# Kernel optimization log

Hardware: AMD Instinct MI355X
Metric: run time of the kernel (lower is better)

Reference implementation:

```python
import jax, jax.numpy as jnp
import numpy as np

M, K, N = 8192, 4096, 4096


def setup_inputs() -> dict:
    key = jax.random.key(0)
    k1, k2, k3 = jax.random.split(key, 3)
    inp = jax.random.normal(k1, (M, K), dtype=jnp.float32)
    weight = jax.random.normal(k2, (N, K), dtype=jnp.float32)
    bias = jax.random.normal(k3, (N,), dtype=jnp.bfloat16)
    return {"inp": inp, "weight": weight, "bias": bias}


def reference(inp, weight, bias):
    # FP8TensorMeta scales are all ones in the source module.
    scale = jnp.float32(1.0)       # quantization scale
    scale_inv = jnp.float32(1.0)   # dequantization scale (per operand)

    # cast_to_fp8: scale then saturate-cast to e4m3
    inp_fp8 = (inp * scale).astype(jnp.float8_e4m3fn)
    weight_fp8 = (weight * scale).astype(jnp.float8_e4m3fn)

    # fp8_gemm: dequantized GEMM with fp32 accumulation, bf16 bias, fp32 out
    out = jnp.einsum(
        "mk,nk->mn",
        inp_fp8.astype(jnp.float32),
        weight_fp8.astype(jnp.float32),
    ) * (scale_inv * scale_inv)
    out = out + bias.astype(jnp.float32)[None, :]
    return out
```

## Files before the change

### kernel.cpp

```cpp
#include <hip/hip_runtime.h>
#include <hip/hip_bf16.h>
#include <stdint.h>


#define MD 8192
#define KD 4096
#define ND 4096
#define BM 128
#define BN 128
#define BK 64

using f32x4 = __attribute__((ext_vector_type(4))) float;

__global__ __launch_bounds__(256) void quant_fp8_fused_kernel(
    const float* __restrict__ inA, const float* __restrict__ inW,
    uint8_t* __restrict__ outA, uint8_t* __restrict__ outW) {
  const int NA4 = MD * KD / 4;
  const int NW4 = ND * KD / 4;
  const int tid = blockIdx.x * blockDim.x + threadIdx.x;
  const int stride = gridDim.x * blockDim.x;

  for (int i = tid; i < NA4; i += stride) {
    float4 f = ((const float4*)inA)[i];
    int v = 0;
    v = __builtin_amdgcn_cvt_pk_fp8_f32(f.x, f.y, v, false);
    v = __builtin_amdgcn_cvt_pk_fp8_f32(f.z, f.w, v, true);
    ((int*)outA)[i] = v;
  }
  for (int i = tid; i < NW4; i += stride) {
    float4 f = ((const float4*)inW)[i];
    int v = 0;
    v = __builtin_amdgcn_cvt_pk_fp8_f32(f.x, f.y, v, false);
    v = __builtin_amdgcn_cvt_pk_fp8_f32(f.z, f.w, v, true);
    ((int*)outW)[i] = v;
  }
}

__device__ __forceinline__ void gload16(const uint8_t* g, uint8_t* l) {
  __builtin_amdgcn_global_load_lds(
      (const __attribute__((address_space(1))) void*)g,
      (__attribute__((address_space(3))) void*)l, 16, 0, 0);
}

__global__ __launch_bounds__(256, 2) void fp8_gemm_bias_kernel(
    const uint8_t* __restrict__ A, const uint8_t* __restrict__ B,
    const __hip_bfloat16* __restrict__ bias, float* __restrict__ C) {
  __shared__ uint8_t sm[2][2][BM * BK];

  const int bid = blockIdx.x;
  const int swz = (bid & 7) * (2048 >> 3) + (bid >> 3);
  const int tm = swz >> 5;
  const int tn = swz & 31;

  const int t = threadIdx.x;
  const int w = t >> 6;
  const int l = t & 63;
  const int wm = w >> 1, wn = w & 1;
  const int r16 = l & 15, kg = l >> 4;

  const int row_a = t >> 2;
  const int gsw = (t & 3) ^ ((row_a >> 1) & 3);
  const size_t a0 = (size_t)(tm * BM + row_a) * KD + gsw * 16;
  const size_t a1 = a0 + (size_t)64 * KD;
  const size_t b0 = (size_t)(tn * BN + row_a) * KD + gsw * 16;
  const size_t b1 = b0 + (size_t)64 * KD;
  const int wd = w * 1024;

  const int s = (r16 >> 1) & 3;
  const int kg2 = kg >> 1;
  const int sub8 = (kg & 1) * 8;
  const int abase = (wm * 64 + r16) * 64 + sub8;
  const int bbase = (wn * 64 + r16) * 64 + sub8;
  const int ch0 = (kg2 ^ s) * 16;
  const int ch1 = ((2 | kg2) ^ s) * 16;

  f32x4 acc[4][4];
#pragma unroll
  for (int m = 0; m < 4; ++m)
#pragma unroll
    for (int n = 0; n < 4; ++n) acc[m][n] = (f32x4){0.f, 0.f, 0.f, 0.f};

  auto stage = [&](int buf, int kt) {
    const size_t ko = (size_t)kt * BK;
    gload16(A + a0 + ko, &sm[buf][0][wd]);
    gload16(A + a1 + ko, &sm[buf][0][4096 + wd]);
    gload16(B + b0 + ko, &sm[buf][1][wd]);
    gload16(B + b1 + ko, &sm[buf][1][4096 + wd]);
  };

  auto compute = [&](int buf) {
    const uint8_t* sa = &sm[buf][0][0];
    const uint8_t* sb = &sm[buf][1][0];
#pragma unroll
    for (int kc = 0; kc < 2; ++kc) {
      const int ch = kc ? ch1 : ch0;
      long long af[4], bf[4];
#pragma unroll
      for (int m = 0; m < 4; ++m)
        af[m] = *(const long long*)(sa + abase + m * 1024 + ch);
#pragma unroll
      for (int n = 0; n < 4; ++n)
        bf[n] = *(const long long*)(sb + bbase + n * 1024 + ch);
#pragma unroll
      for (int m = 0; m < 4; ++m)
#pragma unroll
        for (int n = 0; n < 4; ++n)
          acc[m][n] = __builtin_amdgcn_mfma_f32_16x16x32_fp8_fp8(
              af[m], bf[n], acc[m][n], 0, 0, 0);
    }
  };

  const int NT = KD / BK;
  stage(0, 0);
  __syncthreads();
#pragma unroll 1
  for (int kt = 0; kt < NT - 1; ++kt) {
    const int cur = kt & 1;
    stage(cur ^ 1, kt + 1);
    compute(cur);
    __syncthreads();
  }
  compute((NT - 1) & 1);

  const int gcol = tn * BN + wn * 64 + r16;
  const int grow = tm * BM + wm * 64 + kg * 4;
#pragma unroll
  for (int n = 0; n < 4; ++n) {
    const float bv = __bfloat162float(bias[gcol + n * 16]);
#pragma unroll
    for (int m = 0; m < 4; ++m) {
      const f32x4 v = acc[m][n];
#pragma unroll
      for (int j = 0; j < 4; ++j) {
        C[(size_t)(grow + m * 16 + j) * ND + (gcol + n * 16)] = v[j] + bv;
      }
    }
  }
}

extern "C" void kernel_launch(void* const* d_in, const int* in_sizes, int n_in,
                              void* d_out, int out_size, void* d_ws, size_t ws_size,
                              hipStream_t stream) {
  const float* inp = (const float*)d_in[0];
  const float* wgt = (const float*)d_in[1];
  const __hip_bfloat16* bias = (const __hip_bfloat16*)d_in[2];
  float* out = (float*)d_out;

  uint8_t* a8 = (uint8_t*)d_ws;
  uint8_t* b8 = a8 + (size_t)MD * KD;

  quant_fp8_fused_kernel<<<2048, 256, 0, stream>>>(inp, wgt, a8, b8);
  fp8_gemm_bias_kernel<<<2048, 256, 0, stream>>>(a8, b8, bias, out);
}
```

Measured before the change: 439.1 us.

## Use 32x32x64 scaled MFMA for FP8 GEMM and regroup tile swizzle

Replaces the 16x16x32 FP8 MFMA with the gfx950 32x32x64 f8f6f4 scaled MFMA, using unit scales (0x7F exponent). Each wave now issues four large MFMAs per K tile instead of thirty-two small ones, and reads 16-byte LDS vectors instead of 8-byte ones, with a matching change to the fragment layout and epilogue indexing. Block-to-tile mapping also changes to 4x4 tile groups inside each chunk for better L2 locality. The risks are the new output row mapping and whether the LDS swizzle still avoids bank conflicts under the new access pattern.

```diff
diff --git a/kernel.cpp b/kernel.cpp
--- a/kernel.cpp
+++ b/kernel.cpp
@@ -10,7 +10,10 @@
 #define BN 128
 #define BK 64
 
-using f32x4 = __attribute__((ext_vector_type(4))) float;
+using f32x4  = __attribute__((ext_vector_type(4))) float;
+using f32x16 = __attribute__((ext_vector_type(16))) float;
+using i32x4  = __attribute__((ext_vector_type(4))) int;
+using i32x8  = __attribute__((ext_vector_type(8))) int;
 
 __global__ __launch_bounds__(256) void quant_fp8_fused_kernel(
     const float* __restrict__ inA, const float* __restrict__ inW,
@@ -42,21 +45,23 @@
       (__attribute__((address_space(3))) void*)l, 16, 0, 0);
 }
 
-__global__ __launch_bounds__(256, 2) void fp8_gemm_bias_kernel(
+__global__ __launch_bounds__(256, 2) void fp8mx_gemm_bias_kernel(
     const uint8_t* __restrict__ A, const uint8_t* __restrict__ B,
     const __hip_bfloat16* __restrict__ bias, float* __restrict__ C) {
   __shared__ uint8_t sm[2][2][BM * BK];
 
   const int bid = blockIdx.x;
-  const int swz = (bid & 7) * (2048 >> 3) + (bid >> 3);
-  const int tm = swz >> 5;
-  const int tn = swz & 31;
+  const int chunk = bid & 7;
+  const int local = bid >> 3;
+  const int g = local >> 4, li = local & 15;
+  const int tm = chunk * 8 + (g >> 3) * 4 + (li >> 2);
+  const int tn = (g & 7) * 4 + (li & 3);
 
   const int t = threadIdx.x;
   const int w = t >> 6;
   const int l = t & 63;
   const int wm = w >> 1, wn = w & 1;
-  const int r16 = l & 15, kg = l >> 4;
+  const int r31 = l & 31, kh = l >> 5;
 
   const int row_a = t >> 2;
   const int gsw = (t & 3) ^ ((row_a >> 1) & 3);
@@ -66,19 +71,17 @@
   const size_t b1 = b0 + (size_t)64 * KD;
   const int wd = w * 1024;
 
-  const int s = (r16 >> 1) & 3;
-  const int kg2 = kg >> 1;
-  const int sub8 = (kg & 1) * 8;
-  const int abase = (wm * 64 + r16) * 64 + sub8;
-  const int bbase = (wn * 64 + r16) * 64 + sub8;
-  const int ch0 = (kg2 ^ s) * 16;
-  const int ch1 = ((2 | kg2) ^ s) * 16;
+  const int s = (r31 >> 1) & 3;
+  const int cLo = (((kh << 1) | 0) ^ s) * 16;
+  const int cHi = (((kh << 1) | 1) ^ s) * 16;
 
-  f32x4 acc[4][4];
+  f32x16 acc[2][2];
 #pragma unroll
-  for (int m = 0; m < 4; ++m)
+  for (int fm = 0; fm < 2; ++fm)
 #pragma unroll
-    for (int n = 0; n < 4; ++n) acc[m][n] = (f32x4){0.f, 0.f, 0.f, 0.f};
+    for (int fn = 0; fn < 2; ++fn)
+#pragma unroll
+      for (int r = 0; r < 16; ++r) acc[fm][fn][r] = 0.f;
 
   auto stage = [&](int buf, int kt) {
     const size_t ko = (size_t)kt * BK;
@@ -91,23 +94,30 @@
   auto compute = [&](int buf) {
     const uint8_t* sa = &sm[buf][0][0];
     const uint8_t* sb = &sm[buf][1][0];
+    i32x8 af[2], bf[2];
 #pragma unroll
-    for (int kc = 0; kc < 2; ++kc) {
-      const int ch = kc ? ch1 : ch0;
-      long long af[4], bf[4];
+    for (int f = 0; f < 2; ++f) {
+      const int ra = (wm * 64 + f * 32 + r31) * 64;
+      i32x4 alo = *(const i32x4*)(sa + ra + cLo);
+      i32x4 ahi = *(const i32x4*)(sa + ra + cHi);
+      const int rb = (wn * 64 + f * 32 + r31) * 64;
+      i32x4 blo = *(const i32x4*)(sb + rb + cLo);
+      i32x4 bhi = *(const i32x4*)(sb + rb + cHi);
 #pragma unroll
-      for (int m = 0; m < 4; ++m)
-        af[m] = *(const long long*)(sa + abase + m * 1024 + ch);
+      for (int j = 0; j < 4; ++j) {
+        af[f][j] = alo[j]; af[f][4 + j] = ahi[j];
+        bf[f][j] = blo[j]; bf[f][4 + j] = bhi[j];
+      }
+    }
 #pragma unroll
-      for (int n = 0; n < 4; ++n)
-        bf[n] = *(const long long*)(sb + bbase + n * 1024 + ch);
+    for (int fm = 0; fm < 2; ++fm)
 #pragma unroll
-      for (int m = 0; m < 4; ++m)
-#pragma unroll
-        for (int n = 0; n < 4; ++n)
-          acc[m][n] = __builtin_amdgcn_mfma_f32_16x16x32_fp8_fp8(
-              af[m], bf[n], acc[m][n], 0, 0, 0);
-    }
+      for (int fn = 0; fn < 2; ++fn)
+        acc[fm][fn] = __builtin_amdgcn_mfma_scale_f32_32x32x64_f8f6f4(
+            af[fm], bf[fn], acc[fm][fn],
+            0, 0,
+            0, 0x7F7F7F7F,
+            0, 0x7F7F7F7F);
   };
 
   const int NT = KD / BK;
@@ -122,20 +132,20 @@
   }
   compute((NT - 1) & 1);
 
-  const int gcol = tn * BN + wn * 64 + r16;
-  const int grow = tm * BM + wm * 64 + kg * 4;
 #pragma unroll
-  for (int n = 0; n < 4; ++n) {
-    const float bv = __bfloat162float(bias[gcol + n * 16]);
+  for (int fm = 0; fm < 2; ++fm)
 #pragma unroll
-    for (int m = 0; m < 4; ++m) {
-      const f32x4 v = acc[m][n];
+    for (int fn = 0; fn < 2; ++fn) {
+      const int col = tn * BN + wn * 64 + fn * 32 + r31;
+      const float bv = __bfloat162float(bias[col]);
+      const int row0 = tm * BM + wm * 64 + fm * 32 + 4 * kh;
+      const f32x16 v = acc[fm][fn];
 #pragma unroll
-      for (int j = 0; j < 4; ++j) {
-        C[(size_t)(grow + m * 16 + j) * ND + (gcol + n * 16)] = v[j] + bv;
+      for (int r = 0; r < 16; ++r) {
+        const int row = row0 + (r & 3) + 8 * (r >> 2);
+        C[(size_t)row * ND + col] = v[r] + bv;
       }
     }
-  }
 }
 
 extern "C" void kernel_launch(void* const* d_in, const int* in_sizes, int n_in,
@@ -150,5 +160,5 @@
   uint8_t* b8 = a8 + (size_t)MD * KD;
 
   quant_fp8_fused_kernel<<<2048, 256, 0, stream>>>(inp, wgt, a8, b8);
-  fp8_gemm_bias_kernel<<<2048, 256, 0, stream>>>(a8, b8, bias, out);
+  fp8mx_gemm_bias_kernel<<<2048, 256, 0, stream>>>(a8, b8, bias, out);
 }
```

After: 418.2 us. -4.8%, faster.
